# Kernel optimization log

Measured on AMD Instinct MI355X. Metric: run time of the kernel, lower is better.

The kernel has to match this reference:

```python
import jax, jax.numpy as jnp
import numpy as np

H = 16  # num_heads

def setup_inputs() -> dict:
    key = jax.random.key(0)
    ks = jax.random.split(key, 5)
    d = 1024
    s = 0.02
    return {
        'x': jax.random.normal(ks[0], (2, 2048, d), jnp.float32),
        'Wq': jax.random.normal(ks[1], (d, d), jnp.float32) * s,
        'bq': jnp.zeros((d,), jnp.float32),
        'Wk': jax.random.normal(ks[2], (d, d), jnp.float32) * s,
        'bk': jnp.zeros((d,), jnp.float32),
        'Wv': jax.random.normal(ks[3], (d, d), jnp.float32) * s,
        'bv': jnp.zeros((d,), jnp.float32),
        'Wo': jax.random.normal(ks[4], (d, d), jnp.float32) * s,
        'bo': jnp.zeros((d,), jnp.float32),
        'ln_scale': jnp.ones((d,), jnp.float32),
        'ln_bias': jnp.zeros((d,), jnp.float32),
    }

def _layernorm(x, scale, bias, eps=1e-6):
    mu = jnp.mean(x, axis=-1, keepdims=True)
    var = jnp.var(x, axis=-1, keepdims=True)
    return (x - mu) * jax.lax.rsqrt(var + eps) * scale + bias

def reference(x, Wq, bq, Wk, bk, Wv, bv, Wo, bo, ln_scale, ln_bias):
    b, n, d = x.shape
    hd = d // H
    scale = hd ** -0.5
    residual = x
    xn = _layernorm(x, ln_scale, ln_bias)
    # QKV projections, split heads: [b, n, d] -> [b, H, n, hd]
    def split(y):
        return y.reshape(b, n, H, hd).transpose(0, 2, 1, 3)
    q = split(xn @ Wq + bq)
    k = split(xn @ Wk + bk)
    v = split(xn @ Wv + bv)
    attn = jnp.einsum('bhid,bhjd->bhij', q, k) * scale
    attn = jax.nn.softmax(attn, axis=-1)
    out = jnp.einsum('bhij,bhjd->bhid', attn, v)
    out = out.transpose(0, 2, 1, 3).reshape(b, n, d)
    out = out @ Wo + bo
    return out + residual
```

## Files before the change

kernel.cpp:

```cpp
#include <hip/hip_runtime.h>

typedef __bf16 bf16;
typedef __bf16 bf16x8 __attribute__((ext_vector_type(8)));
typedef float f32x4 __attribute__((ext_vector_type(4)));

#define D_MODEL 1024
#define SEQ 2048
#define NH 16
#define HD 64

#define GLD16(gp, lp) __builtin_amdgcn_global_load_lds( \
    (const __attribute__((address_space(1))) void*)(gp), \
    (__attribute__((address_space(3))) void*)(lp), 16, 0, 0)

__global__ __launch_bounds__(256) void ln_kernel(const float* __restrict__ x,
        const float* __restrict__ g, const float* __restrict__ bta,
        bf16* __restrict__ xnb) {
    int tok = blockIdx.x;
    const float* xr = x + (size_t)tok * D_MODEL;
    float v[4];
    float s = 0.f, ss = 0.f;
#pragma unroll
    for (int j = 0; j < 4; ++j) {
        int idx = threadIdx.x + j * 256;
        float t = xr[idx];
        v[j] = t; s += t; ss += t * t;
    }
#pragma unroll
    for (int m = 32; m; m >>= 1) { s += __shfl_xor(s, m, 64); ss += __shfl_xor(ss, m, 64); }
    __shared__ float red_s[4], red_ss[4];
    int w = threadIdx.x >> 6;
    if ((threadIdx.x & 63) == 0) { red_s[w] = s; red_ss[w] = ss; }
    __syncthreads();
    s  = red_s[0] + red_s[1] + red_s[2] + red_s[3];
    ss = red_ss[0] + red_ss[1] + red_ss[2] + red_ss[3];
    float mu  = s * (1.f / D_MODEL);
    float var = ss * (1.f / D_MODEL) - mu * mu;
    float rstd = rsqrtf(var + 1e-6f);
    bf16* orow = xnb + (size_t)tok * D_MODEL;
#pragma unroll
    for (int j = 0; j < 4; ++j) {
        int idx = threadIdx.x + j * 256;
        float xn = (v[j] - mu) * rstd * g[idx] + bta[idx];
        orow[idx] = (bf16)xn;
    }
}

__global__ __launch_bounds__(256) void transpose_kernel(const float* __restrict__ W0,
        const float* __restrict__ W1, const float* __restrict__ W2,
        const float* __restrict__ W3, bf16* __restrict__ wt) {
    __shared__ float tile[32][33];
    int mat = blockIdx.z;
    const float* W = mat == 0 ? W0 : mat == 1 ? W1 : mat == 2 ? W2 : W3;
    bf16* dst = wt + (size_t)mat * D_MODEL * D_MODEL;
    int k0 = blockIdx.x * 32, n0 = blockIdx.y * 32;
    int tx = threadIdx.x & 31, ty0 = threadIdx.x >> 5;
#pragma unroll
    for (int r = 0; r < 4; ++r) {
        int ty = ty0 + r * 8;
        tile[ty][tx] = W[(size_t)(k0 + ty) * D_MODEL + n0 + tx];
    }
    __syncthreads();
#pragma unroll
    for (int r = 0; r < 4; ++r) {
        int ty = ty0 + r * 8;
        dst[(size_t)(n0 + ty) * D_MODEL + k0 + tx] = (bf16)tile[tx][ty];
    }
}

__global__ __launch_bounds__(256) void qkv_gemm(const bf16* __restrict__ A,
        const bf16* __restrict__ Bt, const float* __restrict__ bq,
        const float* __restrict__ bk, const float* __restrict__ bv,
        bf16* __restrict__ qo, bf16* __restrict__ ko, bf16* __restrict__ vto) {
    __shared__ __align__(16) bf16 As[128 * 32];
    __shared__ __align__(16) bf16 Bs[128 * 32];
    int m0 = blockIdx.x * 128, n0 = blockIdx.y * 128;
    int tid = threadIdx.x;
    int w = tid >> 6, l = tid & 63, lm = l & 15, lq = l >> 4;
    int wm = (w >> 1) * 64, wn = (w & 1) * 64;
    f32x4 acc[4][4] = {};
    const bf16* ag = A  + (size_t)(m0 + w * 32 + (l >> 2)) * D_MODEL + (l & 3) * 8;
    const bf16* bg = Bt + (size_t)(n0 + w * 32 + (l >> 2)) * D_MODEL + (l & 3) * 8;
    bf16* asd = &As[(w * 32) * 32];
    bf16* bsd = &Bs[(w * 32) * 32];
    for (int k0 = 0; k0 < D_MODEL; k0 += 32) {
        GLD16(ag,                asd);
        GLD16(ag + 16 * D_MODEL, asd + 16 * 32);
        GLD16(bg,                bsd);
        GLD16(bg + 16 * D_MODEL, bsd + 16 * 32);
        ag += 32; bg += 32;
        __syncthreads();
        bf16x8 af[4], bf_[4];
#pragma unroll
        for (int f = 0; f < 4; ++f) af[f]  = *(const bf16x8*)&As[(wm + f * 16 + lm) * 32 + lq * 8];
#pragma unroll
        for (int f = 0; f < 4; ++f) bf_[f] = *(const bf16x8*)&Bs[(wn + f * 16 + lm) * 32 + lq * 8];
#pragma unroll
        for (int fm = 0; fm < 4; ++fm)
#pragma unroll
            for (int fn = 0; fn < 4; ++fn)
                acc[fm][fn] = __builtin_amdgcn_mfma_f32_16x16x32_bf16(af[fm], bf_[fn], acc[fm][fn], 0, 0, 0);
        __syncthreads();
    }
#pragma unroll
    for (int fn = 0; fn < 4; ++fn) {
        int n_g = n0 + wn + fn * 16 + lm;
        int mat = n_g >> 10, within = n_g & 1023;
        int h = within >> 6, hdp = within & 63;
        float bias = mat == 0 ? bq[within] : mat == 1 ? bk[within] : bv[within];
#pragma unroll
        for (int fm = 0; fm < 4; ++fm) {
#pragma unroll
            for (int r = 0; r < 4; ++r) {
                int m_g = m0 + wm + fm * 16 + lq * 4 + r;
                int b_ = m_g >> 11, i = m_g & 2047;
                int bh = b_ * NH + h;
                float val = acc[fm][fn][r] + bias;
                if (mat == 0)      qo [((size_t)bh * SEQ + i) * HD + hdp] = (bf16)(val * 0.125f);
                else if (mat == 1) ko [((size_t)bh * SEQ + i) * HD + hdp] = (bf16)val;
                else               vto[((size_t)bh * HD + hdp) * SEQ + i] = (bf16)val;
            }
        }
    }
}

__global__ __launch_bounds__(256) void attn_kernel(const bf16* __restrict__ q,
        const bf16* __restrict__ k, const bf16* __restrict__ vt,
        bf16* __restrict__ aout) {
    __shared__ __align__(16) bf16 Qs[64][72];
    __shared__ __align__(16) bf16 Ks[64][72];
    __shared__ __align__(16) bf16 Vs[64][72];
    int i0 = blockIdx.x * 64;
    int bh = blockIdx.y;
    int tid = threadIdx.x;
    int ar = tid >> 2, ac = (tid & 3) * 8;
    int w = tid >> 6, l = tid & 63, lm = l & 15, lq = l >> 4;
    int sr = (ar & 0x23) | ((ar & 0x0C) << 1) | ((ar & 0x10) >> 2);
    const bf16* qb = q + (size_t)bh * SEQ * HD;
    const bf16* kb = k + (size_t)bh * SEQ * HD;
    const bf16* vb = vt + (size_t)bh * HD * SEQ;
#pragma unroll
    for (int cc = 0; cc < 2; ++cc) {
        int col = ac + cc * 32;
        *(uint4*)&Qs[ar][col] = *(const uint4*)(qb + (size_t)(i0 + ar) * HD + col);
    }
    __syncthreads();
    bf16x8 qf[2];
    qf[0] = *(const bf16x8*)&Qs[w * 16 + lm][lq * 8];
    qf[1] = *(const bf16x8*)&Qs[w * 16 + lm][32 + lq * 8];

    f32x4 o[4] = {};
    float l_acc = 0.f;

    for (int j0 = 0; j0 < SEQ; j0 += 64) {
#pragma unroll
        for (int cc = 0; cc < 2; ++cc) {
            int col = ac + cc * 32;
            *(uint4*)&Ks[ar][col] = *(const uint4*)(kb + (size_t)(j0 + sr) * HD + col);
            *(uint4*)&Vs[ar][col] = *(const uint4*)(vb + (size_t)ar * SEQ + j0 + col);
        }
        __syncthreads();
        f32x4 s[4] = {};
#pragma unroll
        for (int kc = 0; kc < 2; ++kc) {
#pragma unroll
            for (int nt = 0; nt < 4; ++nt) {
                bf16x8 kf = *(const bf16x8*)&Ks[nt * 16 + lm][kc * 32 + lq * 8];
                s[nt] = __builtin_amdgcn_mfma_f32_16x16x32_bf16(kf, qf[kc], s[nt], 0, 0, 0);
            }
        }
        float psum = 0.f;
#pragma unroll
        for (int nt = 0; nt < 4; ++nt)
#pragma unroll
            for (int r = 0; r < 4; ++r) {
                float p = __expf(s[nt][r]);
                s[nt][r] = p; psum += p;
            }
        l_acc += psum;
#pragma unroll
        for (int kc = 0; kc < 2; ++kc) {
            bf16x8 pf;
#pragma unroll
            for (int jj = 0; jj < 8; ++jj)
                pf[jj] = (bf16)s[2 * kc + (jj >> 2)][jj & 3];
#pragma unroll
            for (int nt = 0; nt < 4; ++nt) {
                bf16x8 vf = *(const bf16x8*)&Vs[nt * 16 + lm][kc * 32 + lq * 8];
                o[nt] = __builtin_amdgcn_mfma_f32_16x16x32_bf16(pf, vf, o[nt], 0, 0, 0);
            }
        }
        __syncthreads();
    }
    l_acc += __shfl_xor(l_acc, 16, 64);
    l_acc += __shfl_xor(l_acc, 32, 64);
    float linv[4];
#pragma unroll
    for (int r = 0; r < 4; ++r)
        linv[r] = 1.f / __shfl(l_acc, lq * 4 + r, 64);
    int b_ = bh >> 4, h = bh & 15;
#pragma unroll
    for (int nt = 0; nt < 4; ++nt) {
#pragma unroll
        for (int r = 0; r < 4; ++r) {
            int i = i0 + w * 16 + lq * 4 + r;
            int tok = b_ * SEQ + i;
            aout[(size_t)tok * D_MODEL + h * HD + nt * 16 + lm] = (bf16)(o[nt][r] * linv[r]);
        }
    }
}

__global__ __launch_bounds__(256) void out_gemm(const bf16* __restrict__ A,
        const bf16* __restrict__ Bt, const float* __restrict__ bo,
        const float* __restrict__ resid, float* __restrict__ out) {
    __shared__ __align__(16) bf16 As[128 * 32];
    __shared__ __align__(16) bf16 Bs[128 * 32];
    int m0 = blockIdx.x * 128, n0 = blockIdx.y * 128;
    int tid = threadIdx.x;
    int w = tid >> 6, l = tid & 63, lm = l & 15, lq = l >> 4;
    int wm = (w >> 1) * 64, wn = (w & 1) * 64;
    f32x4 acc[4][4] = {};
    const bf16* ag = A  + (size_t)(m0 + w * 32 + (l >> 2)) * D_MODEL + (l & 3) * 8;
    const bf16* bg = Bt + (size_t)(n0 + w * 32 + (l >> 2)) * D_MODEL + (l & 3) * 8;
    bf16* asd = &As[(w * 32) * 32];
    bf16* bsd = &Bs[(w * 32) * 32];
    for (int k0 = 0; k0 < D_MODEL; k0 += 32) {
        GLD16(ag,                asd);
        GLD16(ag + 16 * D_MODEL, asd + 16 * 32);
        GLD16(bg,                bsd);
        GLD16(bg + 16 * D_MODEL, bsd + 16 * 32);
        ag += 32; bg += 32;
        __syncthreads();
        bf16x8 af[4], bf_[4];
#pragma unroll
        for (int f = 0; f < 4; ++f) af[f]  = *(const bf16x8*)&As[(wm + f * 16 + lm) * 32 + lq * 8];
#pragma unroll
        for (int f = 0; f < 4; ++f) bf_[f] = *(const bf16x8*)&Bs[(wn + f * 16 + lm) * 32 + lq * 8];
#pragma unroll
        for (int fm = 0; fm < 4; ++fm)
#pragma unroll
            for (int fn = 0; fn < 4; ++fn)
                acc[fm][fn] = __builtin_amdgcn_mfma_f32_16x16x32_bf16(af[fm], bf_[fn], acc[fm][fn], 0, 0, 0);
        __syncthreads();
    }
#pragma unroll
    for (int fn = 0; fn < 4; ++fn) {
        int n_g = n0 + wn + fn * 16 + lm;
        float bias = bo[n_g];
#pragma unroll
        for (int fm = 0; fm < 4; ++fm) {
#pragma unroll
            for (int r = 0; r < 4; ++r) {
                int m_g = m0 + wm + fm * 16 + lq * 4 + r;
                size_t idx = (size_t)m_g * D_MODEL + n_g;
                out[idx] = acc[fm][fn][r] + bias + resid[idx];
            }
        }
    }
}

extern "C" void kernel_launch(void* const* d_in, const int* in_sizes, int n_in,
                              void* d_out, int out_size, void* d_ws, size_t ws_size,
                              hipStream_t stream) {
    const float* x  = (const float*)d_in[0];
    const float* Wq = (const float*)d_in[1];
    const float* bq = (const float*)d_in[2];
    const float* Wk = (const float*)d_in[3];
    const float* bk = (const float*)d_in[4];
    const float* Wv = (const float*)d_in[5];
    const float* bv = (const float*)d_in[6];
    const float* Wo = (const float*)d_in[7];
    const float* bo = (const float*)d_in[8];
    const float* g  = (const float*)d_in[9];
    const float* bt = (const float*)d_in[10];
    (void)in_sizes; (void)n_in; (void)out_size; (void)ws_size;

    char* ws = (char*)d_ws;
    const size_t M8 = (size_t)8 << 20;
    bf16* xnb = (bf16*)(ws);
    bf16* wt  = (bf16*)(ws + M8);
    bf16* qb  = (bf16*)(ws + 2 * M8);
    bf16* kb  = (bf16*)(ws + 3 * M8);
    bf16* vtb = (bf16*)(ws + 4 * M8);
    bf16* ao  = xnb;
    float* out = (float*)d_out;

    ln_kernel<<<4096, 256, 0, stream>>>(x, g, bt, xnb);
    transpose_kernel<<<dim3(32, 32, 4), 256, 0, stream>>>(Wq, Wk, Wv, Wo, wt);
    qkv_gemm<<<dim3(32, 24), 256, 0, stream>>>(xnb, wt, bq, bk, bv, qb, kb, vtb);
    attn_kernel<<<dim3(32, 32), 256, 0, stream>>>(qb, kb, vtb, ao);
    out_gemm<<<dim3(32, 8), 256, 0, stream>>>(ao, wt + (size_t)3 * D_MODEL * D_MODEL, bo, x, out);
}
```

Measured before the change: 226.1 us.

## Double query tile per attention block, async LDS loads with XOR swizzle, exp2 softmax

The attention kernel now handles 128 queries per block, so each wave keeps two 16-row query fragments and reuses every K/V fragment it reads from LDS across both. K and V tiles are fetched with global_load_lds straight into an XOR-swizzled unpadded layout, which replaces register-staged copies and is meant to avoid bank conflicts. The Q scale now includes log2(e) so the softmax can call exp2f. The grid is halved, which lowers the number of blocks available to spread across CUs, and register use goes up.

```diff
diff --git a/kernel.cpp b/kernel.cpp
--- a/kernel.cpp
+++ b/kernel.cpp
@@ -12,6 +12,10 @@
 #define GLD16(gp, lp) __builtin_amdgcn_global_load_lds( \
     (const __attribute__((address_space(1))) void*)(gp), \
     (__attribute__((address_space(3))) void*)(lp), 16, 0, 0)
+
+__device__ __forceinline__ int sigp(int r) {
+    return (r & 0x23) | ((r & 0x0C) << 1) | ((r & 0x10) >> 2);
+}
 
 __global__ __launch_bounds__(256) void ln_kernel(const float* __restrict__ x,
         const float* __restrict__ g, const float* __restrict__ bta,
@@ -116,7 +120,7 @@
                 int b_ = m_g >> 11, i = m_g & 2047;
                 int bh = b_ * NH + h;
                 float val = acc[fm][fn][r] + bias;
-                if (mat == 0)      qo [((size_t)bh * SEQ + i) * HD + hdp] = (bf16)(val * 0.125f);
+                if (mat == 0)      qo [((size_t)bh * SEQ + i) * HD + hdp] = (bf16)(val * 0.180336888f);
                 else if (mat == 1) ko [((size_t)bh * SEQ + i) * HD + hdp] = (bf16)val;
                 else               vto[((size_t)bh * HD + hdp) * SEQ + i] = (bf16)val;
             }
@@ -127,85 +131,112 @@
 __global__ __launch_bounds__(256) void attn_kernel(const bf16* __restrict__ q,
         const bf16* __restrict__ k, const bf16* __restrict__ vt,
         bf16* __restrict__ aout) {
-    __shared__ __align__(16) bf16 Qs[64][72];
-    __shared__ __align__(16) bf16 Ks[64][72];
-    __shared__ __align__(16) bf16 Vs[64][72];
-    int i0 = blockIdx.x * 64;
+    __shared__ __align__(16) bf16 Qs[128][72];
+    __shared__ __align__(16) bf16 Ks[64 * 64];
+    __shared__ __align__(16) bf16 Vs[64 * 64];
+    int i0 = blockIdx.x * 128;
     int bh = blockIdx.y;
     int tid = threadIdx.x;
-    int ar = tid >> 2, ac = (tid & 3) * 8;
     int w = tid >> 6, l = tid & 63, lm = l & 15, lq = l >> 4;
-    int sr = (ar & 0x23) | ((ar & 0x0C) << 1) | ((ar & 0x10) >> 2);
     const bf16* qb = q + (size_t)bh * SEQ * HD;
     const bf16* kb = k + (size_t)bh * SEQ * HD;
     const bf16* vb = vt + (size_t)bh * HD * SEQ;
-#pragma unroll
-    for (int cc = 0; cc < 2; ++cc) {
-        int col = ac + cc * 32;
-        *(uint4*)&Qs[ar][col] = *(const uint4*)(qb + (size_t)(i0 + ar) * HD + col);
-    }
+
+    {
+        int tr = tid >> 1, half = tid & 1;
+#pragma unroll
+        for (int c = 0; c < 4; ++c) {
+            int col = half * 32 + c * 8;
+            *(uint4*)&Qs[tr][col] = *(const uint4*)(qb + (size_t)(i0 + tr) * HD + col);
+        }
+    }
+    int row0 = w * 16 + (l >> 3);
+    int g = l & 7;
+    const bf16* ks0 = kb + (size_t)sigp(row0) * HD     + (size_t)((g ^ (row0 & 7)) * 8);
+    const bf16* ks1 = kb + (size_t)sigp(row0 + 8) * HD + (size_t)((g ^ ((row0 + 8) & 7)) * 8);
+    const bf16* vs0 = vb + (size_t)row0 * SEQ       + (size_t)((g ^ (row0 & 7)) * 8);
+    const bf16* vs1 = vb + (size_t)(row0 + 8) * SEQ + (size_t)((g ^ ((row0 + 8) & 7)) * 8);
+    bf16* kd0 = &Ks[(w * 16) * 64];
+    bf16* kd1 = &Ks[(w * 16 + 8) * 64];
+    bf16* vd0 = &Vs[(w * 16) * 64];
+    bf16* vd1 = &Vs[(w * 16 + 8) * 64];
+
     __syncthreads();
-    bf16x8 qf[2];
-    qf[0] = *(const bf16x8*)&Qs[w * 16 + lm][lq * 8];
-    qf[1] = *(const bf16x8*)&Qs[w * 16 + lm][32 + lq * 8];
-
-    f32x4 o[4] = {};
-    float l_acc = 0.f;
+    bf16x8 qf[2][2];
+#pragma unroll
+    for (int mf = 0; mf < 2; ++mf)
+#pragma unroll
+        for (int kc = 0; kc < 2; ++kc)
+            qf[mf][kc] = *(const bf16x8*)&Qs[w * 32 + mf * 16 + lm][kc * 32 + lq * 8];
+
+    f32x4 o[2][4] = {};
+    float l_acc[2] = {0.f, 0.f};
 
     for (int j0 = 0; j0 < SEQ; j0 += 64) {
-#pragma unroll
-        for (int cc = 0; cc < 2; ++cc) {
-            int col = ac + cc * 32;
-            *(uint4*)&Ks[ar][col] = *(const uint4*)(kb + (size_t)(j0 + sr) * HD + col);
-            *(uint4*)&Vs[ar][col] = *(const uint4*)(vb + (size_t)ar * SEQ + j0 + col);
-        }
-        __syncthreads();
-        f32x4 s[4] = {};
+        GLD16(ks0, kd0); GLD16(ks1, kd1);
+        GLD16(vs0, vd0); GLD16(vs1, vd1);
+        ks0 += 64 * HD; ks1 += 64 * HD; vs0 += 64; vs1 += 64;
+        __syncthreads();
+        f32x4 s[2][4] = {};
 #pragma unroll
         for (int kc = 0; kc < 2; ++kc) {
 #pragma unroll
             for (int nt = 0; nt < 4; ++nt) {
-                bf16x8 kf = *(const bf16x8*)&Ks[nt * 16 + lm][kc * 32 + lq * 8];
-                s[nt] = __builtin_amdgcn_mfma_f32_16x16x32_bf16(kf, qf[kc], s[nt], 0, 0, 0);
-            }
-        }
-        float psum = 0.f;
-#pragma unroll
-        for (int nt = 0; nt < 4; ++nt)
+                int r = nt * 16 + lm;
+                int gl = (kc * 4 + lq) ^ (lm & 7);
+                bf16x8 kf = *(const bf16x8*)&Ks[r * 64 + gl * 8];
+                s[0][nt] = __builtin_amdgcn_mfma_f32_16x16x32_bf16(kf, qf[0][kc], s[0][nt], 0, 0, 0);
+                s[1][nt] = __builtin_amdgcn_mfma_f32_16x16x32_bf16(kf, qf[1][kc], s[1][nt], 0, 0, 0);
+            }
+        }
+#pragma unroll
+        for (int mf = 0; mf < 2; ++mf) {
+            float psum = 0.f;
+#pragma unroll
+            for (int nt = 0; nt < 4; ++nt)
+#pragma unroll
+                for (int r = 0; r < 4; ++r) {
+                    float p = exp2f(s[mf][nt][r]);
+                    s[mf][nt][r] = p; psum += p;
+                }
+            l_acc[mf] += psum;
+        }
+#pragma unroll
+        for (int kc = 0; kc < 2; ++kc) {
+            bf16x8 pf[2];
+#pragma unroll
+            for (int mf = 0; mf < 2; ++mf)
+#pragma unroll
+                for (int jj = 0; jj < 8; ++jj)
+                    pf[mf][jj] = (bf16)s[mf][2 * kc + (jj >> 2)][jj & 3];
+#pragma unroll
+            for (int nt = 0; nt < 4; ++nt) {
+                int p = nt * 16 + lm;
+                int gl = (kc * 4 + lq) ^ (lm & 7);
+                bf16x8 vf = *(const bf16x8*)&Vs[p * 64 + gl * 8];
+                o[0][nt] = __builtin_amdgcn_mfma_f32_16x16x32_bf16(pf[0], vf, o[0][nt], 0, 0, 0);
+                o[1][nt] = __builtin_amdgcn_mfma_f32_16x16x32_bf16(pf[1], vf, o[1][nt], 0, 0, 0);
+            }
+        }
+        __syncthreads();
+    }
+    int b_ = bh >> 4, h = bh & 15;
+#pragma unroll
+    for (int mf = 0; mf < 2; ++mf) {
+        l_acc[mf] += __shfl_xor(l_acc[mf], 16, 64);
+        l_acc[mf] += __shfl_xor(l_acc[mf], 32, 64);
+        float linv[4];
+#pragma unroll
+        for (int r = 0; r < 4; ++r)
+            linv[r] = 1.f / __shfl(l_acc[mf], lq * 4 + r, 64);
+#pragma unroll
+        for (int nt = 0; nt < 4; ++nt) {
 #pragma unroll
             for (int r = 0; r < 4; ++r) {
-                float p = __expf(s[nt][r]);
-                s[nt][r] = p; psum += p;
-            }
-        l_acc += psum;
-#pragma unroll
-        for (int kc = 0; kc < 2; ++kc) {
-            bf16x8 pf;
-#pragma unroll
-            for (int jj = 0; jj < 8; ++jj)
-                pf[jj] = (bf16)s[2 * kc + (jj >> 2)][jj & 3];
-#pragma unroll
-            for (int nt = 0; nt < 4; ++nt) {
-                bf16x8 vf = *(const bf16x8*)&Vs[nt * 16 + lm][kc * 32 + lq * 8];
-                o[nt] = __builtin_amdgcn_mfma_f32_16x16x32_bf16(pf, vf, o[nt], 0, 0, 0);
-            }
-        }
-        __syncthreads();
-    }
-    l_acc += __shfl_xor(l_acc, 16, 64);
-    l_acc += __shfl_xor(l_acc, 32, 64);
-    float linv[4];
-#pragma unroll
-    for (int r = 0; r < 4; ++r)
-        linv[r] = 1.f / __shfl(l_acc, lq * 4 + r, 64);
-    int b_ = bh >> 4, h = bh & 15;
-#pragma unroll
-    for (int nt = 0; nt < 4; ++nt) {
-#pragma unroll
-        for (int r = 0; r < 4; ++r) {
-            int i = i0 + w * 16 + lq * 4 + r;
-            int tok = b_ * SEQ + i;
-            aout[(size_t)tok * D_MODEL + h * HD + nt * 16 + lm] = (bf16)(o[nt][r] * linv[r]);
+                int i = i0 + w * 32 + mf * 16 + lq * 4 + r;
+                int tok = b_ * SEQ + i;
+                aout[(size_t)tok * D_MODEL + h * HD + nt * 16 + lm] = (bf16)(o[mf][nt][r] * linv[r]);
+            }
         }
     }
 }
@@ -288,6 +319,6 @@
     ln_kernel<<<4096, 256, 0, stream>>>(x, g, bt, xnb);
     transpose_kernel<<<dim3(32, 32, 4), 256, 0, stream>>>(Wq, Wk, Wv, Wo, wt);
     qkv_gemm<<<dim3(32, 24), 256, 0, stream>>>(xnb, wt, bq, bk, bv, qb, kb, vtb);
-    attn_kernel<<<dim3(32, 32), 256, 0, stream>>>(qb, kb, vtb, ao);
+    attn_kernel<<<dim3(16, 32), 256, 0, stream>>>(qb, kb, vtb, ao);
     out_gemm<<<dim3(32, 8), 256, 0, stream>>>(ao, wt + (size_t)3 * D_MODEL * D_MODEL, bo, x, out);
 }
```

After: 222.9 us. No clear change (-1.4%).
